# Optimization experiments

Hardware: AMD Instinct MI355X
Metric: run time of the kernel (lower is better)

Reference implementation:

```python
import jax, jax.numpy as jnp
import numpy as np

B, N, D, L = 32, 512, 768, 4  # batch, nodes (incl. CLS at last index), in_dim==hidden_size, num_layers


def setup_inputs() -> dict:
    key = jax.random.key(0)
    ks = jax.random.split(key, 6)
    feature = jax.random.normal(ks[0], (B, N, D), jnp.float32)
    # token mask: random valid lengths, CLS node at the last index always present
    lengths = jax.random.randint(ks[1], (B,), N // 2, N)
    pmask = (jnp.arange(N)[None, :] < lengths[:, None]).astype(jnp.float32)
    pmask = pmask.at[:, -1].set(1.0)
    # L2C (learning-to-connect) bilinear gate params, one pair per layer
    Wq = jax.random.normal(ks[2], (L, D, D), jnp.float32) / np.sqrt(D)
    Wk = jax.random.normal(ks[3], (L, D, D), jnp.float32) / np.sqrt(D)
    # attention-pool projection Linear(in_dim, 1)
    proj_w = jax.random.normal(ks[4], (D,), jnp.float32) / np.sqrt(D)
    proj_b = jnp.zeros((), jnp.float32)
    return dict(pmask=pmask, feature=feature, Wq=Wq, Wk=Wk, proj_w=proj_w, proj_b=proj_b)


def reference(pmask, feature, Wq, Wk, proj_w, proj_b):
    full_adj = pmask[:, :, None] * pmask[:, None, :]        # [B,N,N]
    full_sum = jnp.sum(full_adj) + 1e-8
    p_sum = pmask.sum(-1)                                    # [B]
    scale = 1.0 / np.sqrt(D)
    preds = [feature]
    adjs, c_list, g_list = [], [], []
    total_l0 = jnp.zeros((), feature.dtype)
    for l in range(L):
        # L2C: bilinear sigmoid gate masked by full adjacency, L0-style loss = mean gate mass
        q = jnp.einsum('bnd,de->bne', feature, Wq[l])
        k = jnp.einsum('bnd,de->bne', feature, Wk[l])
        adj = jax.nn.sigmoid(jnp.einsum('bne,bme->bnm', q, k) * scale) * full_adj  # [B,N,N]
        total_l0 = total_l0 + jnp.sum(adj) / full_sum
        # sparse_statistics: CLS-row sparsity and graph-edge sparsity
        c_list.append(adj[:, -1, :-1].sum(-1) / p_sum)               # [B]
        g_list.append(adj[:, :-1, :-1].sum((-1, -2)) / p_sum ** 2)   # [B]
        adjs.append(adj)
        # symmetric degree normalization: D^-1/2 A D^-1/2 (diag bmm == row/col scaling)
        deg = adj.sum(2)                                              # [B,N]
        dis = jnp.where(deg > 0, jax.lax.rsqrt(jnp.maximum(deg, 1e-12)), 0.0)
        dis = jax.lax.stop_gradient(dis)                              # .detach() in original
        adj_n = dis[:, :, None] * adj * dis[:, None, :]
        # feature = adj_^T @ feature
        feature = jnp.einsum('bnm,bnd->bmd', adj_n, feature)
        preds.append(feature)
    pps = jnp.stack(preds, axis=2)                                    # [B,N,L+1,D]
    retain = jax.nn.sigmoid(jnp.einsum('bnld,d->bnl', pps, proj_w) + proj_b)  # [B,N,L+1]
    out = jnp.einsum('bnl,bnld->bnd', retain, pps)                    # [B,N,D]
    c_sparsity = jnp.stack(c_list, axis=-1)                           # [B,L]
    g_sparsity = jnp.stack(g_list, axis=-1)                           # [B,L]
    return (out, retain, jnp.stack(adjs, axis=-1), total_l0 / L, c_sparsity, g_sparsity)
```

## Files before the change

### kernel.cpp

```cpp
#include <hip/hip_runtime.h>

typedef short s16x8 __attribute__((ext_vector_type(8)));
typedef float f32x4 __attribute__((ext_vector_type(4)));

constexpr int BATCH = 32, NODES = 512, DIM = 768, LAYERS = 4;
constexpr float QK_SCALE = 0.03608439182435161f;

constexpr size_t OUT_OFF  = 0;
constexpr size_t RET_OFF  = (size_t)BATCH * NODES * DIM;
constexpr size_t ADJS_OFF = RET_OFF + (size_t)BATCH * NODES * (LAYERS + 1);
constexpr size_t L0_OFF   = ADJS_OFF + (size_t)BATCH * NODES * NODES * LAYERS;
constexpr size_t C_OFF    = L0_OFF + 1;
constexpr size_t G_OFF    = C_OFF + BATCH * LAYERS;

#define DEVI static __device__ __forceinline__

DEVI float bf2f(unsigned short u) {
    union { unsigned int i; float f; } v; v.i = ((unsigned int)u) << 16; return v.f;
}
DEVI unsigned short f2bf(float f) {
    union { float f; unsigned int i; } v; v.f = f;
    return (unsigned short)((v.i + 0x7FFFu + ((v.i >> 16) & 1u)) >> 16);
}
DEVI ushort4 pk4(float4 v) {
    ushort4 o; o.x = f2bf(v.x); o.y = f2bf(v.y); o.z = f2bf(v.z); o.w = f2bf(v.w); return o;
}
DEVI float sigm(float x) { return 1.0f / (1.0f + __expf(-x)); }
DEVI float deg2dis(float d) { return d > 0.f ? rsqrtf(fmaxf(d, 1e-12f)) : 0.f; }

DEVI void gload16(const unsigned short* g, unsigned short* l) {
    __builtin_amdgcn_global_load_lds(
        (const __attribute__((address_space(1))) unsigned int*)g,
        (__attribute__((address_space(3))) unsigned int*)l, 16, 0, 0);
}

template <int MODE>
__global__ __launch_bounds__(256) void gemm_nt(
    const unsigned short* __restrict__ A0, const unsigned short* __restrict__ B0,
    unsigned short* __restrict__ C0,
    int K, int lda, int ldb, int ldc,
    long sA, long sB, long sC,
    const float* __restrict__ pmask, float* __restrict__ deg,
    unsigned short* __restrict__ adjT,
    float* __restrict__ l0_acc, float* __restrict__ c_acc, float* __restrict__ g_acc,
    int layer)
{
    __shared__ __align__(16) unsigned short As[128 * 32];
    __shared__ __align__(16) unsigned short Bs[128 * 32];

    const int tid  = threadIdx.x;
    const int lane = tid & 63;
    const int wave = tid >> 6;
    const int wr = (wave >> 1) << 6;
    const int wc = (wave & 1) << 6;
    const int z = blockIdx.z;
    const int rows0 = blockIdx.x << 7;
    const int cols0 = blockIdx.y << 7;

    const unsigned short* A = A0 + (size_t)z * sA + (size_t)rows0 * lda;
    const unsigned short* Bsrc = B0 + (size_t)z * sB + (size_t)cols0 * ldb;

    f32x4 acc[4][4] = {};

    const int srow = wave * 16 + (lane >> 2);
    const int scb  = (lane & 3) << 3;
    const unsigned short* Ag = A + (size_t)srow * lda + scb;
    const unsigned short* Bg = Bsrc + (size_t)srow * ldb + scb;
    unsigned short* lA0 = &As[wave * 512];
    unsigned short* lA1 = &As[2048 + wave * 512];
    unsigned short* lB0 = &Bs[wave * 512];
    unsigned short* lB1 = &Bs[2048 + wave * 512];
    const size_t a64 = (size_t)64 * lda, b64 = (size_t)64 * ldb;

    const int mrow = lane & 15;
    const int kq   = (lane >> 4) << 3;

    for (int kt = 0; kt < K; kt += 32) {
        __syncthreads();
        gload16(Ag + kt, lA0);
        gload16(Ag + a64 + kt, lA1);
        gload16(Bg + kt, lB0);
        gload16(Bg + b64 + kt, lB1);
        __syncthreads();

        s16x8 af[4], bfr[4];
        #pragma unroll
        for (int i = 0; i < 4; ++i) {
            af[i]  = *(const s16x8*)(&As[(wr + i * 16 + mrow) * 32 + kq]);
            bfr[i] = *(const s16x8*)(&Bs[(wc + i * 16 + mrow) * 32 + kq]);
        }
        #pragma unroll
        for (int i = 0; i < 4; ++i)
            #pragma unroll
            for (int j = 0; j < 4; ++j)
                acc[i][j] = __builtin_amdgcn_mfma_f32_16x16x32_bf16(af[i], bfr[j], acc[i][j], 0, 0, 0);
    }

    const int colb = lane & 15, quad = lane >> 4;
    unsigned short* C = C0 + (size_t)z * sC;
    #pragma unroll
    for (int i = 0; i < 4; ++i) {
        const int rbase = rows0 + wr + i * 16 + (quad << 2);
        #pragma unroll
        for (int j = 0; j < 4; ++j) {
            const int cc = cols0 + wc + j * 16 + colb;
            #pragma unroll
            for (int r = 0; r < 4; ++r)
                C[(size_t)(rbase + r) * ldc + cc] = f2bf(acc[i][j][r]);
        }
    }
}

template <int MODE>
__global__ __launch_bounds__(512) void gemm256_nt(
    const unsigned short* __restrict__ A0, const unsigned short* __restrict__ B0,
    unsigned short* __restrict__ C0,
    int K, int lda, int ldb, int ldc,
    long sA, long sB, long sC,
    const float* __restrict__ pmask, float* __restrict__ deg,
    unsigned short* __restrict__ adjT,
    float* __restrict__ l0_acc, float* __restrict__ c_acc, float* __restrict__ g_acc,
    int layer)
{
    __shared__ __align__(16) unsigned short lds[2][2][2][8192];
    __shared__ float pmr[256];
    __shared__ float pmc[256];

    const int tid  = threadIdx.x;
    const int lane = tid & 63;
    const int wave = tid >> 6;
    const int wm   = wave >> 2;
    const int wn   = wave & 3;
    const int z = blockIdx.z;
    const int rows0 = blockIdx.x << 8;
    const int cols0 = blockIdx.y << 8;

    const unsigned short* A = A0 + (size_t)z * sA;
    const unsigned short* B = B0 + (size_t)z * sB;

    if constexpr (MODE == 1) {
        if (tid < 256) pmr[tid] = pmask[(size_t)z * NODES + rows0 + tid];
        else pmc[tid - 256] = pmask[(size_t)z * NODES + cols0 + (tid - 256)];
    }

    const int srow  = lane >> 3;
    const int scol8 = (lane & 7) ^ srow;

    auto stage_half = [&](int T, int op, int h) {
        const int base = (op == 0) ? rows0 : cols0;
        const int ld   = (op == 0) ? lda : ldb;
        const unsigned short* src = ((op == 0) ? A : B)
            + (size_t)(base + h * 128 + wave * 8 + srow) * ld + (size_t)T * 64 + scol8 * 8;
        unsigned short* dst = &lds[T & 1][op][h][wave * 512];
        gload16(src, dst);
        gload16(src + (size_t)64 * ld, dst + 4096);
    };

    const int nkt = K >> 6;

    stage_half(0, 0, 0); stage_half(0, 0, 1);
    stage_half(0, 1, 0); stage_half(0, 1, 1);
    if (nkt > 1) {
        stage_half(1, 0, 0);
        asm volatile("s_waitcnt vmcnt(2)" ::: "memory");
    } else {
        asm volatile("s_waitcnt vmcnt(0)" ::: "memory");
    }
    __builtin_amdgcn_s_barrier();
    asm volatile("" ::: "memory");

    f32x4 acc[8][4] = {};

    const int fr = lane & 15;
    const int fq = lane >> 4;
    const int xk = (fr & 7) << 4;
    const int frow64 = fr * 64;
    const int ka0 = ((fq * 16) ^ xk) >> 1;
    const int ka1 = ((64 + fq * 16) ^ xk) >> 1;
    const int brow = (wn & 1) * 4096;

    for (int T = 0; T < nkt; ++T) {
        const unsigned short* Ah = &lds[T & 1][0][wm][0];
        const unsigned short* Bh = &lds[T & 1][1][wn >> 1][0];
        s16x8 af[4][2], bq[4][2];

        #pragma unroll
        for (int i = 0; i < 4; ++i) {
            af[i][0] = *(const s16x8*)(Ah + i * 1024 + frow64 + ka0);
            af[i][1] = *(const s16x8*)(Ah + i * 1024 + frow64 + ka1);
        }
        #pragma unroll
        for (int j = 0; j < 2; ++j) {
            bq[j][0] = *(const s16x8*)(Bh + brow + j * 1024 + frow64 + ka0);
            bq[j][1] = *(const s16x8*)(Bh + brow + j * 1024 + frow64 + ka1);
        }
        if (T + 1 < nkt) stage_half(T + 1, 0, 1);
        asm volatile("" ::: "memory");
        __builtin_amdgcn_s_barrier();
        asm volatile("s_waitcnt lgkmcnt(0)" ::: "memory");
        __builtin_amdgcn_sched_barrier(0);
        __builtin_amdgcn_s_setprio(1);
        #pragma unroll
        for (int i = 0; i < 4; ++i)
            #pragma unroll
            for (int j = 0; j < 2; ++j)
                #pragma unroll
                for (int s = 0; s < 2; ++s)
                    acc[i][j] = __builtin_amdgcn_mfma_f32_16x16x32_bf16(af[i][s], bq[j][s], acc[i][j], 0, 0, 0);
        __builtin_amdgcn_s_setprio(0);
        asm volatile("" ::: "memory");
        __builtin_amdgcn_s_barrier();
        asm volatile("" ::: "memory");

        #pragma unroll
        for (int j = 0; j < 2; ++j) {
            bq[2 + j][0] = *(const s16x8*)(Bh + brow + (2 + j) * 1024 + frow64 + ka0);
            bq[2 + j][1] = *(const s16x8*)(Bh + brow + (2 + j) * 1024 + frow64 + ka1);
        }
        if (T + 1 < nkt) stage_half(T + 1, 1, 0);
        asm volatile("" ::: "memory");
        __builtin_amdgcn_s_barrier();
        asm volatile("s_waitcnt lgkmcnt(0)" ::: "memory");
        __builtin_amdgcn_sched_barrier(0);
        __builtin_amdgcn_s_setprio(1);
        #pragma unroll
        for (int i = 0; i < 4; ++i)
            #pragma unroll
            for (int j = 2; j < 4; ++j)
                #pragma unroll
                for (int s = 0; s < 2; ++s)
                    acc[i][j] = __builtin_amdgcn_mfma_f32_16x16x32_bf16(af[i][s], bq[j][s], acc[i][j], 0, 0, 0);
        __builtin_amdgcn_s_setprio(0);
        asm volatile("" ::: "memory");
        __builtin_amdgcn_s_barrier();
        asm volatile("" ::: "memory");

        #pragma unroll
        for (int i = 0; i < 4; ++i) {
            af[i][0] = *(const s16x8*)(Ah + (4 + i) * 1024 + frow64 + ka0);
            af[i][1] = *(const s16x8*)(Ah + (4 + i) * 1024 + frow64 + ka1);
        }
        if (T + 1 < nkt) stage_half(T + 1, 1, 1);
        asm volatile("" ::: "memory");
        __builtin_amdgcn_s_barrier();
        asm volatile("s_waitcnt lgkmcnt(0)" ::: "memory");
        __builtin_amdgcn_sched_barrier(0);
        __builtin_amdgcn_s_setprio(1);
        #pragma unroll
        for (int i = 0; i < 4; ++i)
            #pragma unroll
            for (int j = 2; j < 4; ++j)
                #pragma unroll
                for (int s = 0; s < 2; ++s)
                    acc[4 + i][j] = __builtin_amdgcn_mfma_f32_16x16x32_bf16(af[i][s], bq[j][s], acc[4 + i][j], 0, 0, 0);
        __builtin_amdgcn_s_setprio(0);
        asm volatile("" ::: "memory");
        __builtin_amdgcn_s_barrier();
        asm volatile("" ::: "memory");

        if (T + 2 < nkt) stage_half(T + 2, 0, 0);
        asm volatile("" ::: "memory");
        __builtin_amdgcn_s_barrier();
        asm volatile("" ::: "memory");
        __builtin_amdgcn_s_setprio(1);
        #pragma unroll
        for (int i = 0; i < 4; ++i)
            #pragma unroll
            for (int j = 0; j < 2; ++j)
                #pragma unroll
                for (int s = 0; s < 2; ++s)
                    acc[4 + i][j] = __builtin_amdgcn_mfma_f32_16x16x32_bf16(af[i][s], bq[j][s], acc[4 + i][j], 0, 0, 0);
        __builtin_amdgcn_s_setprio(0);
        if (T + 2 < nkt) asm volatile("s_waitcnt vmcnt(2)" ::: "memory");
        else             asm volatile("s_waitcnt vmcnt(0)" ::: "memory");
        __builtin_amdgcn_s_barrier();
        asm volatile("" ::: "memory");
    }

    const int quad4 = fq << 2;

    if constexpr (MODE != 1) {
        unsigned short* C = C0 + (size_t)z * sC;
        #pragma unroll
        for (int i = 0; i < 8; ++i) {
            const int rbase = rows0 + wm * 128 + i * 16 + quad4;
            float dv[4];
            if constexpr (MODE == 2) {
                #pragma unroll
                for (int r = 0; r < 4; ++r) dv[r] = deg2dis(deg[(size_t)z * NODES + rbase + r]);
            }
            #pragma unroll
            for (int j = 0; j < 4; ++j) {
                const int cc = cols0 + wn * 64 + j * 16 + fr;
                #pragma unroll
                for (int r = 0; r < 4; ++r) {
                    float v = acc[i][j][r];
                    if constexpr (MODE == 2) v *= dv[r];
                    C[(size_t)(rbase + r) * ldc + cc] = f2bf(v);
                }
            }
        }
    } else {
        float tot = 0.f, gs = 0.f, cs = 0.f;
        #pragma unroll
        for (int i = 0; i < 8; ++i) {
            const int nloc = wm * 128 + i * 16 + quad4;
            #pragma unroll
            for (int r = 0; r < 4; ++r) {
                const int n = rows0 + nloc + r;
                const float pmn = pmr[nloc + r];
                float dp = 0.f;
                #pragma unroll
                for (int j = 0; j < 4; ++j) {
                    const int mloc = wn * 64 + j * 16 + fr;
                    const int m = cols0 + mloc;
                    float a = pmn * pmc[mloc] * sigm(acc[i][j][r] * QK_SCALE);
                    acc[i][j][r] = a;
                    dp += a;
                    tot += a;
                    if (m < NODES - 1) {
                        if (n < NODES - 1) gs += a;
                        else cs += a;
                    }
                }
                dp += __shfl_xor(dp, 1, 16);
                dp += __shfl_xor(dp, 2, 16);
                dp += __shfl_xor(dp, 4, 16);
                dp += __shfl_xor(dp, 8, 16);
                if (fr == 0) atomicAdd(&deg[(size_t)z * NODES + n], dp);
            }
        }
        #pragma unroll
        for (int i = 0; i < 8; ++i) {
            const int nb = rows0 + wm * 128 + i * 16 + quad4;
            #pragma unroll
            for (int j = 0; j < 4; ++j) {
                const int m = cols0 + wn * 64 + j * 16 + fr;
                ushort4 pk;
                pk.x = f2bf(acc[i][j][0]); pk.y = f2bf(acc[i][j][1]);
                pk.z = f2bf(acc[i][j][2]); pk.w = f2bf(acc[i][j][3]);
                *(ushort4*)(adjT + ((size_t)z * NODES + m) * NODES + nb) = pk;
            }
        }
        #pragma unroll
        for (int o = 1; o < 64; o <<= 1) {
            tot += __shfl_xor(tot, o, 64);
            gs  += __shfl_xor(gs, o, 64);
            cs  += __shfl_xor(cs, o, 64);
        }
        if (lane == 0) {
            atomicAdd(l0_acc, tot);
            atomicAdd(&g_acc[z * LAYERS + layer], gs);
            atomicAdd(&c_acc[z * LAYERS + layer], cs);
        }
    }
}

__global__ __launch_bounds__(256) void interleave_adjs(
    const unsigned short* __restrict__ adjT, float* __restrict__ adjs)
{
    __shared__ unsigned short t[4][32][36];
    const int b = blockIdx.z, m0 = blockIdx.x << 5, n0 = blockIdx.y << 5;
    const int tr = threadIdx.x >> 3, tc = (threadIdx.x & 7) << 2;
    #pragma unroll
    for (int l = 0; l < LAYERS; ++l) {
        ushort4 v = *(const ushort4*)(adjT + (((size_t)l * BATCH + b) * NODES + m0 + tr) * NODES + n0 + tc);
        t[l][tr][tc] = v.x; t[l][tr][tc + 1] = v.y; t[l][tr][tc + 2] = v.z; t[l][tr][tc + 3] = v.w;
    }
    __syncthreads();
    float* dst = adjs + (((size_t)b * NODES + n0 + tr) * NODES + m0 + tc) * LAYERS;
    #pragma unroll
    for (int mm = 0; mm < 4; ++mm) {
        float4 f;
        f.x = bf2f(t[0][tc + mm][tr]); f.y = bf2f(t[1][tc + mm][tr]);
        f.z = bf2f(t[2][tc + mm][tr]); f.w = bf2f(t[3][tc + mm][tr]);
        *(float4*)(dst + mm * 4) = f;
    }
}

__global__ void fp_transpose(const unsigned short* __restrict__ X, const float* __restrict__ deg,
                             unsigned short* __restrict__ fpt)
{
    __shared__ unsigned short t[32][36];
    const int b = blockIdx.z;
    const int n0 = blockIdx.x << 5, d0 = blockIdx.y << 5;
    const int tr = threadIdx.x >> 3, tc = (threadIdx.x & 7) << 2;
    const float dv = deg2dis(deg[(size_t)b * NODES + n0 + tr]);
    ushort4 v = *(const ushort4*)(X + ((size_t)b * NODES + n0 + tr) * DIM + d0 + tc);
    t[tr][tc]     = f2bf(bf2f(v.x) * dv);
    t[tr][tc + 1] = f2bf(bf2f(v.y) * dv);
    t[tr][tc + 2] = f2bf(bf2f(v.z) * dv);
    t[tr][tc + 3] = f2bf(bf2f(v.w) * dv);
    __syncthreads();
    ushort4 o;
    o.x = t[tc + 0][tr]; o.y = t[tc + 1][tr]; o.z = t[tc + 2][tr]; o.w = t[tc + 3][tr];
    *(ushort4*)(fpt + ((size_t)b * DIM + d0 + tr) * NODES + n0 + tc) = o;
}

__global__ void cast_all(const float* __restrict__ feat, const float* __restrict__ Wq,
                         const float* __restrict__ Wk, unsigned short* __restrict__ featb,
                         unsigned short* __restrict__ Wqb, unsigned short* __restrict__ Wkb)
{
    const int bx = blockIdx.x;
    const float* src; unsigned short* dst; size_t base;
    if (bx < 12288)      { src = feat; dst = featb; base = (size_t)bx * 1024; }
    else if (bx < 14592) { src = Wq;   dst = Wqb;   base = (size_t)(bx - 12288) * 1024; }
    else                 { src = Wk;   dst = Wkb;   base = (size_t)(bx - 14592) * 1024; }
    const size_t i = base + ((size_t)threadIdx.x << 2);
    float4 v = *(const float4*)(src + i);
    *(ushort4*)(dst + i) = pk4(v);
}

__global__ void psum_kernel(const float* __restrict__ pm, float* __restrict__ ps)
{
    const int b = blockIdx.x, t = threadIdx.x;
    float s = pm[(size_t)b * NODES + t] + pm[(size_t)b * NODES + 256 + t];
    #pragma unroll
    for (int o = 1; o < 64; o <<= 1) s += __shfl_xor(s, o, 64);
    __shared__ float sh[4];
    if ((t & 63) == 0) sh[t >> 6] = s;
    __syncthreads();
    if (t == 0) ps[b] = sh[0] + sh[1] + sh[2] + sh[3];
}

__global__ __launch_bounds__(256) void final_out(
    const float* __restrict__ X0f, const unsigned short* __restrict__ X1,
    const unsigned short* __restrict__ X2, const unsigned short* __restrict__ X3,
    const unsigned short* __restrict__ X4,
    const float* __restrict__ pw, const float* __restrict__ pb,
    const float* __restrict__ ps, const float* __restrict__ c_acc,
    const float* __restrict__ g_acc, const float* __restrict__ l0,
    float* __restrict__ ob)
{
    if (blockIdx.x == 0) {
        const int t = threadIdx.x;
        if (t < BATCH * LAYERS) {
            const int b = t >> 2;
            const float p = ps[b];
            ob[C_OFF + t] = c_acc[t] / p;
            ob[G_OFF + t] = g_acc[t] / (p * p);
        }
        if (t == 0) {
            float fs = 1e-8f;
            for (int b = 0; b < BATCH; ++b) fs += ps[b] * ps[b];
            ob[L0_OFF] = l0[0] / (fs * (float)LAYERS);
        }
    }

    const int row = (blockIdx.x << 2) + (threadIdx.x >> 6);
    const int lane = threadIdx.x & 63;
    const unsigned short* Xb[4] = { X1 + (size_t)row * DIM, X2 + (size_t)row * DIM,
                                    X3 + (size_t)row * DIM, X4 + (size_t)row * DIM };
    float xs[5][12];
    float dot[5] = {};
    #pragma unroll
    for (int c = 0; c < 3; ++c) {
        const int idx = c * 256 + (lane << 2);
        float4 wv = *(const float4*)(pw + idx);
        float4 x0 = *(const float4*)(X0f + (size_t)row * DIM + idx);
        xs[0][c * 4 + 0] = x0.x; xs[0][c * 4 + 1] = x0.y;
        xs[0][c * 4 + 2] = x0.z; xs[0][c * 4 + 3] = x0.w;
        dot[0] += x0.x * wv.x + x0.y * wv.y + x0.z * wv.z + x0.w * wv.w;
        #pragma unroll
        for (int l = 0; l < 4; ++l) {
            ushort4 xv = *(const ushort4*)(Xb[l] + idx);
            float a0 = bf2f(xv.x), a1 = bf2f(xv.y), a2 = bf2f(xv.z), a3 = bf2f(xv.w);
            xs[l + 1][c * 4 + 0] = a0; xs[l + 1][c * 4 + 1] = a1;
            xs[l + 1][c * 4 + 2] = a2; xs[l + 1][c * 4 + 3] = a3;
            dot[l + 1] += a0 * wv.x + a1 * wv.y + a2 * wv.z + a3 * wv.w;
        }
    }
    #pragma unroll
    for (int l = 0; l < 5; ++l)
        #pragma unroll
        for (int o = 1; o < 64; o <<= 1) dot[l] += __shfl_xor(dot[l], o, 64);
    const float pbv = pb[0];
    float r[5];
    #pragma unroll
    for (int l = 0; l < 5; ++l) r[l] = sigm(dot[l] + pbv);
    if (lane == 0) {
        float* rr = ob + RET_OFF + (size_t)row * (LAYERS + 1);
        rr[0] = r[0]; rr[1] = r[1]; rr[2] = r[2]; rr[3] = r[3]; rr[4] = r[4];
    }
    float* orow = ob + OUT_OFF + (size_t)row * DIM;
    #pragma unroll
    for (int c = 0; c < 3; ++c) {
        float4 p;
        p.x = r[0] * xs[0][c * 4 + 0]; p.y = r[0] * xs[0][c * 4 + 1];
        p.z = r[0] * xs[0][c * 4 + 2]; p.w = r[0] * xs[0][c * 4 + 3];
        #pragma unroll
        for (int l = 1; l < 5; ++l) {
            p.x += r[l] * xs[l][c * 4 + 0]; p.y += r[l] * xs[l][c * 4 + 1];
            p.z += r[l] * xs[l][c * 4 + 2]; p.w += r[l] * xs[l][c * 4 + 3];
        }
        *(float4*)(orow + c * 256 + (lane << 2)) = p;
    }
}

extern "C" void kernel_launch(void* const* d_in, const int* in_sizes, int n_in,
                              void* d_out, int out_size, void* d_ws, size_t ws_size,
                              hipStream_t stream)
{
    (void)in_sizes; (void)n_in; (void)out_size; (void)ws_size;
    const float* pmask = (const float*)d_in[0];
    const float* feat  = (const float*)d_in[1];
    const float* Wq    = (const float*)d_in[2];
    const float* Wk    = (const float*)d_in[3];
    const float* projw = (const float*)d_in[4];
    const float* projb = (const float*)d_in[5];
    float* ob = (float*)d_out;

    char* w = (char*)d_ws;
    unsigned short* Xb[4];
    Xb[0] = (unsigned short*)(w + 0);
    Xb[1] = (unsigned short*)(w + 25165824);
    Xb[2] = (unsigned short*)(w + 50331648);
    Xb[3] = (unsigned short*)(w + 75497472);
    unsigned short* qws   = (unsigned short*)(w + 100663296);
    unsigned short* featb = (unsigned short*)(w + 125829120);
    unsigned short* adjT  = (unsigned short*)(w + 150994944);
    unsigned short* Wqb   = (unsigned short*)(w + 218103808);
    unsigned short* Wkb   = (unsigned short*)(w + 222822400);
    unsigned short* MT    = (unsigned short*)(w + 227540992);
    float* deg_all = (float*)(w + 232259584);
    float* c_acc   = (float*)(w + 232521728);
    float* g_acc   = (float*)(w + 232522240);
    float* l0_acc  = (float*)(w + 232522752);
    float* p_sum   = (float*)(w + 232523008);

    dim3 blk(256);
    dim3 blk5(512);
    hipMemsetAsync(w + 232259584, 0, 263680, stream);

    cast_all<<<dim3(16896), blk, 0, stream>>>(feat, Wq, Wk, featb, Wqb, Wkb);
    psum_kernel<<<dim3(32), blk, 0, stream>>>(pmask, p_sum);

    gemm_nt<0><<<dim3(6, 6, 4), blk, 0, stream>>>(
        Wkb, Wqb, MT, DIM, DIM, DIM, DIM,
        (long)DIM * DIM, (long)DIM * DIM, (long)DIM * DIM,
        nullptr, nullptr, nullptr, nullptr, nullptr, nullptr, 0);

    for (int l = 0; l < LAYERS; ++l) {
        float* deg_l = deg_all + (size_t)l * BATCH * NODES;
        unsigned short* adjT_l = adjT + (size_t)l * BATCH * NODES * NODES;
        const unsigned short* Xsrc = (l == 0) ? featb : Xb[l - 1];

        gemm256_nt<0><<<dim3(64, 3, 1), blk5, 0, stream>>>(
            Xsrc, MT + (size_t)l * DIM * DIM, qws,
            DIM, DIM, DIM, DIM, 0L, 0L, 0L,
            nullptr, nullptr, nullptr, nullptr, nullptr, nullptr, 0);

        gemm256_nt<1><<<dim3(2, 2, 32), blk5, 0, stream>>>(
            qws, Xsrc, nullptr,
            DIM, DIM, DIM, 0, (long)NODES * DIM, (long)NODES * DIM, 0L,
            pmask, deg_l, adjT_l, l0_acc, c_acc, g_acc, l);

        fp_transpose<<<dim3(16, 24, 32), blk, 0, stream>>>(Xsrc, deg_l, qws);

        gemm256_nt<2><<<dim3(2, 3, 32), blk5, 0, stream>>>(
            adjT_l, qws, Xb[l],
            NODES, NODES, NODES, DIM, (long)NODES * NODES, (long)DIM * NODES, (long)NODES * DIM,
            nullptr, deg_l, nullptr, nullptr, nullptr, nullptr, 0);
    }

    interleave_adjs<<<dim3(16, 16, 32), blk, 0, stream>>>(adjT, ob + ADJS_OFF);
    final_out<<<dim3(4096), blk, 0, stream>>>(feat, Xb[0], Xb[1], Xb[2], Xb[3],
                                              projw, projb, p_sum, c_acc, g_acc, l0_acc, ob);
}
```

Before: 782.6 us.

## Shrink main GEMM tile to 128x256 and fold psum into cast kernel

The 256x256 bf16 MFMA GEMM is changed to a 128x256 tile with half the accumulators, a 3-slot LDS layout, and a pipeline of two compute phases per k-step instead of four. Grids double in the row dimension, giving more blocks for the batched 512x512 per-batch GEMMs, which previously launched only 128 or 192 blocks. The pmask row-sum kernel is merged into the cast kernel as extra blocks to save one launch. The smaller tile lowers register pressure and improves occupancy and wave balance, at the cost of less data reuse per block and more global traffic.

```diff
diff --git a/kernel.cpp b/kernel.cpp
--- a/kernel.cpp
+++ b/kernel.cpp
@@ -34,16 +34,11 @@
         (__attribute__((address_space(3))) unsigned int*)l, 16, 0, 0);
 }
 
-template <int MODE>
-__global__ __launch_bounds__(256) void gemm_nt(
+__global__ __launch_bounds__(256) void gemm_nt_small(
     const unsigned short* __restrict__ A0, const unsigned short* __restrict__ B0,
     unsigned short* __restrict__ C0,
     int K, int lda, int ldb, int ldc,
-    long sA, long sB, long sC,
-    const float* __restrict__ pmask, float* __restrict__ deg,
-    unsigned short* __restrict__ adjT,
-    float* __restrict__ l0_acc, float* __restrict__ c_acc, float* __restrict__ g_acc,
-    int layer)
+    long sA, long sB, long sC)
 {
     __shared__ __align__(16) unsigned short As[128 * 32];
     __shared__ __align__(16) unsigned short Bs[128 * 32];
@@ -112,7 +107,7 @@
 }
 
 template <int MODE>
-__global__ __launch_bounds__(512) void gemm256_nt(
+__global__ __launch_bounds__(512) void gemm128_nt(
     const unsigned short* __restrict__ A0, const unsigned short* __restrict__ B0,
     unsigned short* __restrict__ C0,
     int K, int lda, int ldb, int ldc,
@@ -122,8 +117,8 @@
     float* __restrict__ l0_acc, float* __restrict__ c_acc, float* __restrict__ g_acc,
     int layer)
 {
-    __shared__ __align__(16) unsigned short lds[2][2][2][8192];
-    __shared__ float pmr[256];
+    __shared__ __align__(16) unsigned short lds[2][3][8192];
+    __shared__ float pmr[128];
     __shared__ float pmc[256];
 
     const int tid  = threadIdx.x;
@@ -132,44 +127,39 @@
     const int wm   = wave >> 2;
     const int wn   = wave & 3;
     const int z = blockIdx.z;
-    const int rows0 = blockIdx.x << 8;
+    const int rows0 = blockIdx.x << 7;
     const int cols0 = blockIdx.y << 8;
 
     const unsigned short* A = A0 + (size_t)z * sA;
     const unsigned short* B = B0 + (size_t)z * sB;
 
     if constexpr (MODE == 1) {
-        if (tid < 256) pmr[tid] = pmask[(size_t)z * NODES + rows0 + tid];
-        else pmc[tid - 256] = pmask[(size_t)z * NODES + cols0 + (tid - 256)];
+        if (tid < 128) pmr[tid] = pmask[(size_t)z * NODES + rows0 + tid];
+        else if (tid < 384) pmc[tid - 128] = pmask[(size_t)z * NODES + cols0 + (tid - 128)];
     }
 
     const int srow  = lane >> 3;
     const int scol8 = (lane & 7) ^ srow;
 
-    auto stage_half = [&](int T, int op, int h) {
-        const int base = (op == 0) ? rows0 : cols0;
-        const int ld   = (op == 0) ? lda : ldb;
-        const unsigned short* src = ((op == 0) ? A : B)
-            + (size_t)(base + h * 128 + wave * 8 + srow) * ld + (size_t)T * 64 + scol8 * 8;
-        unsigned short* dst = &lds[T & 1][op][h][wave * 512];
-        gload16(src, dst);
-        gload16(src + (size_t)64 * ld, dst + 4096);
+    auto stage = [&](int T, int slot) {
+        const unsigned short* g;
+        size_t ld;
+        if (slot == 0) { g = A + (size_t)(rows0 + wave * 8 + srow) * lda; ld = lda; }
+        else           { g = B + (size_t)(cols0 + (slot - 1) * 128 + wave * 8 + srow) * ldb; ld = ldb; }
+        g += (size_t)T * 64 + scol8 * 8;
+        unsigned short* dst = &lds[T & 1][slot][wave * 512];
+        gload16(g, dst);
+        gload16(g + 64 * ld, dst + 4096);
     };
 
     const int nkt = K >> 6;
 
-    stage_half(0, 0, 0); stage_half(0, 0, 1);
-    stage_half(0, 1, 0); stage_half(0, 1, 1);
-    if (nkt > 1) {
-        stage_half(1, 0, 0);
-        asm volatile("s_waitcnt vmcnt(2)" ::: "memory");
-    } else {
-        asm volatile("s_waitcnt vmcnt(0)" ::: "memory");
-    }
+    stage(0, 0); stage(0, 1); stage(0, 2);
+    asm volatile("s_waitcnt vmcnt(0)" ::: "memory");
     __builtin_amdgcn_s_barrier();
     asm volatile("" ::: "memory");
 
-    f32x4 acc[8][4] = {};
+    f32x4 acc[4][4] = {};
 
     const int fr = lane & 15;
     const int fq = lane >> 4;
@@ -177,11 +167,12 @@
     const int frow64 = fr * 64;
     const int ka0 = ((fq * 16) ^ xk) >> 1;
     const int ka1 = ((64 + fq * 16) ^ xk) >> 1;
-    const int brow = (wn & 1) * 4096;
+    const int abase = wm * 4096;
+    const int brow  = (wn & 1) * 4096;
 
     for (int T = 0; T < nkt; ++T) {
-        const unsigned short* Ah = &lds[T & 1][0][wm][0];
-        const unsigned short* Bh = &lds[T & 1][1][wn >> 1][0];
+        const unsigned short* Ah = &lds[T & 1][0][abase];
+        const unsigned short* Bh = &lds[T & 1][1 + (wn >> 1)][brow];
         s16x8 af[4][2], bq[4][2];
 
         #pragma unroll
@@ -191,10 +182,10 @@
         }
         #pragma unroll
         for (int j = 0; j < 2; ++j) {
-            bq[j][0] = *(const s16x8*)(Bh + brow + j * 1024 + frow64 + ka0);
-            bq[j][1] = *(const s16x8*)(Bh + brow + j * 1024 + frow64 + ka1);
-        }
-        if (T + 1 < nkt) stage_half(T + 1, 0, 1);
+            bq[j][0] = *(const s16x8*)(Bh + j * 1024 + frow64 + ka0);
+            bq[j][1] = *(const s16x8*)(Bh + j * 1024 + frow64 + ka1);
+        }
+        if (T + 1 < nkt) { stage(T + 1, 0); stage(T + 1, 1); }
         asm volatile("" ::: "memory");
         __builtin_amdgcn_s_barrier();
         asm volatile("s_waitcnt lgkmcnt(0)" ::: "memory");
@@ -213,11 +204,12 @@
         asm volatile("" ::: "memory");
 
         #pragma unroll
-        for (int j = 0; j < 2; ++j) {
-            bq[2 + j][0] = *(const s16x8*)(Bh + brow + (2 + j) * 1024 + frow64 + ka0);
-            bq[2 + j][1] = *(const s16x8*)(Bh + brow + (2 + j) * 1024 + frow64 + ka1);
-        }
-        if (T + 1 < nkt) stage_half(T + 1, 1, 0);
+        for (int j = 2; j < 4; ++j) {
+            bq[j][0] = *(const s16x8*)(Bh + j * 1024 + frow64 + ka0);
+            bq[j][1] = *(const s16x8*)(Bh + j * 1024 + frow64 + ka1);
+        }
+        if (T + 1 < nkt) stage(T + 1, 2);
+        if (T + 2 < nkt) stage(T + 2, 0);
         asm volatile("" ::: "memory");
         __builtin_amdgcn_s_barrier();
         asm volatile("s_waitcnt lgkmcnt(0)" ::: "memory");
@@ -231,46 +223,6 @@
                 for (int s = 0; s < 2; ++s)
                     acc[i][j] = __builtin_amdgcn_mfma_f32_16x16x32_bf16(af[i][s], bq[j][s], acc[i][j], 0, 0, 0);
         __builtin_amdgcn_s_setprio(0);
-        asm volatile("" ::: "memory");
-        __builtin_amdgcn_s_barrier();
-        asm volatile("" ::: "memory");
-
-        #pragma unroll
-        for (int i = 0; i < 4; ++i) {
-            af[i][0] = *(const s16x8*)(Ah + (4 + i) * 1024 + frow64 + ka0);
-            af[i][1] = *(const s16x8*)(Ah + (4 + i) * 1024 + frow64 + ka1);
-        }
-        if (T + 1 < nkt) stage_half(T + 1, 1, 1);
-        asm volatile("" ::: "memory");
-        __builtin_amdgcn_s_barrier();
-        asm volatile("s_waitcnt lgkmcnt(0)" ::: "memory");
-        __builtin_amdgcn_sched_barrier(0);
-        __builtin_amdgcn_s_setprio(1);
-        #pragma unroll
-        for (int i = 0; i < 4; ++i)
-            #pragma unroll
-            for (int j = 2; j < 4; ++j)
-                #pragma unroll
-                for (int s = 0; s < 2; ++s)
-                    acc[4 + i][j] = __builtin_amdgcn_mfma_f32_16x16x32_bf16(af[i][s], bq[j][s], acc[4 + i][j], 0, 0, 0);
-        __builtin_amdgcn_s_setprio(0);
-        asm volatile("" ::: "memory");
-        __builtin_amdgcn_s_barrier();
-        asm volatile("" ::: "memory");
-
-        if (T + 2 < nkt) stage_half(T + 2, 0, 0);
-        asm volatile("" ::: "memory");
-        __builtin_amdgcn_s_barrier();
-        asm volatile("" ::: "memory");
-        __builtin_amdgcn_s_setprio(1);
-        #pragma unroll
-        for (int i = 0; i < 4; ++i)
-            #pragma unroll
-            for (int j = 0; j < 2; ++j)
-                #pragma unroll
-                for (int s = 0; s < 2; ++s)
-                    acc[4 + i][j] = __builtin_amdgcn_mfma_f32_16x16x32_bf16(af[i][s], bq[j][s], acc[4 + i][j], 0, 0, 0);
-        __builtin_amdgcn_s_setprio(0);
         if (T + 2 < nkt) asm volatile("s_waitcnt vmcnt(2)" ::: "memory");
         else             asm volatile("s_waitcnt vmcnt(0)" ::: "memory");
         __builtin_amdgcn_s_barrier();
@@ -282,8 +234,8 @@
     if constexpr (MODE != 1) {
         unsigned short* C = C0 + (size_t)z * sC;
         #pragma unroll
-        for (int i = 0; i < 8; ++i) {
-            const int rbase = rows0 + wm * 128 + i * 16 + quad4;
+        for (int i = 0; i < 4; ++i) {
+            const int rbase = rows0 + wm * 64 + i * 16 + quad4;
             float dv[4];
             if constexpr (MODE == 2) {
                 #pragma unroll
@@ -303,8 +255,8 @@
     } else {
         float tot = 0.f, gs = 0.f, cs = 0.f;
         #pragma unroll
-        for (int i = 0; i < 8; ++i) {
-            const int nloc = wm * 128 + i * 16 + quad4;
+        for (int i = 0; i < 4; ++i) {
+            const int nloc = wm * 64 + i * 16 + quad4;
             #pragma unroll
             for (int r = 0; r < 4; ++r) {
                 const int n = rows0 + nloc + r;
@@ -331,8 +283,8 @@
             }
         }
         #pragma unroll
-        for (int i = 0; i < 8; ++i) {
-            const int nb = rows0 + wm * 128 + i * 16 + quad4;
+        for (int i = 0; i < 4; ++i) {
+            const int nb = rows0 + wm * 64 + i * 16 + quad4;
             #pragma unroll
             for (int j = 0; j < 4; ++j) {
                 const int m = cols0 + wn * 64 + j * 16 + fr;
@@ -399,9 +351,21 @@
 
 __global__ void cast_all(const float* __restrict__ feat, const float* __restrict__ Wq,
                          const float* __restrict__ Wk, unsigned short* __restrict__ featb,
-                         unsigned short* __restrict__ Wqb, unsigned short* __restrict__ Wkb)
+                         unsigned short* __restrict__ Wqb, unsigned short* __restrict__ Wkb,
+                         const float* __restrict__ pm, float* __restrict__ ps)
 {
     const int bx = blockIdx.x;
+    if (bx >= 16896) {
+        const int b = bx - 16896, t = threadIdx.x;
+        float s = pm[(size_t)b * NODES + t] + pm[(size_t)b * NODES + 256 + t];
+        #pragma unroll
+        for (int o = 1; o < 64; o <<= 1) s += __shfl_xor(s, o, 64);
+        __shared__ float sh[4];
+        if ((t & 63) == 0) sh[t >> 6] = s;
+        __syncthreads();
+        if (t == 0) ps[b] = sh[0] + sh[1] + sh[2] + sh[3];
+        return;
+    }
     const float* src; unsigned short* dst; size_t base;
     if (bx < 12288)      { src = feat; dst = featb; base = (size_t)bx * 1024; }
     else if (bx < 14592) { src = Wq;   dst = Wqb;   base = (size_t)(bx - 12288) * 1024; }
@@ -409,18 +373,6 @@
     const size_t i = base + ((size_t)threadIdx.x << 2);
     float4 v = *(const float4*)(src + i);
     *(ushort4*)(dst + i) = pk4(v);
-}
-
-__global__ void psum_kernel(const float* __restrict__ pm, float* __restrict__ ps)
-{
-    const int b = blockIdx.x, t = threadIdx.x;
-    float s = pm[(size_t)b * NODES + t] + pm[(size_t)b * NODES + 256 + t];
-    #pragma unroll
-    for (int o = 1; o < 64; o <<= 1) s += __shfl_xor(s, o, 64);
-    __shared__ float sh[4];
-    if ((t & 63) == 0) sh[t >> 6] = s;
-    __syncthreads();
-    if (t == 0) ps[b] = sh[0] + sh[1] + sh[2] + sh[3];
 }
 
 __global__ __launch_bounds__(256) void final_out(
@@ -532,32 +484,30 @@
     dim3 blk5(512);
     hipMemsetAsync(w + 232259584, 0, 263680, stream);
 
-    cast_all<<<dim3(16896), blk, 0, stream>>>(feat, Wq, Wk, featb, Wqb, Wkb);
-    psum_kernel<<<dim3(32), blk, 0, stream>>>(pmask, p_sum);
-
-    gemm_nt<0><<<dim3(6, 6, 4), blk, 0, stream>>>(
+    cast_all<<<dim3(16928), blk, 0, stream>>>(feat, Wq, Wk, featb, Wqb, Wkb, pmask, p_sum);
+
+    gemm_nt_small<<<dim3(6, 6, 4), blk, 0, stream>>>(
         Wkb, Wqb, MT, DIM, DIM, DIM, DIM,
-        (long)DIM * DIM, (long)DIM * DIM, (long)DIM * DIM,
-        nullptr, nullptr, nullptr, nullptr, nullptr, nullptr, 0);
+        (long)DIM * DIM, (long)DIM * DIM, (long)DIM * DIM);
 
     for (int l = 0; l < LAYERS; ++l) {
         float* deg_l = deg_all + (size_t)l * BATCH * NODES;
         unsigned short* adjT_l = adjT + (size_t)l * BATCH * NODES * NODES;
         const unsigned short* Xsrc = (l == 0) ? featb : Xb[l - 1];
 
-        gemm256_nt<0><<<dim3(64, 3, 1), blk5, 0, stream>>>(
+        gemm128_nt<0><<<dim3(128, 3, 1), blk5, 0, stream>>>(
             Xsrc, MT + (size_t)l * DIM * DIM, qws,
             DIM, DIM, DIM, DIM, 0L, 0L, 0L,
             nullptr, nullptr, nullptr, nullptr, nullptr, nullptr, 0);
 
-        gemm256_nt<1><<<dim3(2, 2, 32), blk5, 0, stream>>>(
+        gemm128_nt<1><<<dim3(4, 2, 32), blk5, 0, stream>>>(
             qws, Xsrc, nullptr,
             DIM, DIM, DIM, 0, (long)NODES * DIM, (long)NODES * DIM, 0L,
             pmask, deg_l, adjT_l, l0_acc, c_acc, g_acc, l);
 
         fp_transpose<<<dim3(16, 24, 32), blk, 0, stream>>>(Xsrc, deg_l, qws);
 
-        gemm256_nt<2><<<dim3(2, 3, 32), blk5, 0, stream>>>(
+        gemm128_nt<2><<<dim3(4, 3, 32), blk5, 0, stream>>>(
             adjT_l, qws, Xb[l],
             NODES, NODES, NODES, DIM, (long)NODES * NODES, (long)DIM * NODES, (long)NODES * DIM,
             nullptr, deg_l, nullptr, nullptr, nullptr, nullptr, 0);
```

New measurement: 855.5 us. 9.3% more time.
